# Kernel tuning notes

Measured on AMD Instinct MI355X. Metric: run time of the kernel, lower is better.

## Reference

```python
import jax, jax.numpy as jnp
import numpy as np

NUM_HEADS = 8
NUM_POINTS = 4            # sampling points per pillar point
NUM_PILLAR = 4            # points in pillar
SAMPLING_RADIUS = 0.12


def masked_softmax(logits, mask):
    # logits/mask: [B, N, H, P]; softmax over last dim, robust to fully-masked rows
    m = mask.astype(logits.dtype)
    w = jax.nn.softmax(jnp.where(mask, logits, jnp.asarray(-1e9, logits.dtype)), axis=-1) * m
    return w / jnp.clip(jnp.sum(w, axis=-1, keepdims=True), 1e-6)


def grid_sample_bilinear(feat, loc):
    # feat: [G, D, H, W]; loc: [G, Nq, P, 2] normalized to [0,1]
    # matches torch grid_sample(mode='bilinear', padding_mode='zeros', align_corners=False)
    G, D, H, W = feat.shape
    _, Nq, P, _ = loc.shape
    fm = feat.reshape(G, D, H * W).transpose(0, 2, 1)  # [G, HW, D]
    x = loc[..., 0] * W - 0.5
    y = loc[..., 1] * H - 0.5
    x0 = jnp.floor(x)
    y0 = jnp.floor(y)
    wx = x - x0
    wy = y - y0
    out = jnp.zeros((G, Nq * P, D), dtype=feat.dtype)
    corners = [(0, 0, (1 - wx) * (1 - wy)), (1, 0, wx * (1 - wy)),
               (0, 1, (1 - wx) * wy), (1, 1, wx * wy)]
    for dx, dy, w in corners:
        xi = x0 + dx
        yi = y0 + dy
        valid = (xi >= 0) & (xi < W) & (yi >= 0) & (yi < H)
        xc = jnp.clip(xi, 0, W - 1).astype(jnp.int32)
        yc = jnp.clip(yi, 0, H - 1).astype(jnp.int32)
        idx = (yc * W + xc).reshape(G, Nq * P)
        g = jnp.take_along_axis(fm, idx[:, :, None], axis=1)  # [G, Nq*P, D]
        out = out + g * (w * valid.astype(feat.dtype)).reshape(G, Nq * P, 1)
    return out.reshape(G, Nq, P, D)


def setup_inputs() -> dict:
    key = jax.random.key(0)
    ks = jax.random.split(key, 10)
    B, N, C = 1, 10000, 256
    n_cams, Himg, Wimg = 6, 60, 100
    HD = NUM_HEADS * NUM_PILLAR * NUM_POINTS  # 128
    query = jax.random.normal(ks[0], (B, N, C), jnp.float32)
    image_feats = jax.random.normal(ks[1], (B, n_cams, C, Himg, Wimg), jnp.float32)
    reference_points_cam = jax.random.uniform(ks[2], (B, n_cams, N, NUM_PILLAR, 2), jnp.float32)
    bev_mask = jax.random.bernoulli(ks[3], 0.4, (B, n_cams, N, NUM_PILLAR))
    s = 0.02
    offset_W = jax.random.normal(ks[4], (C, HD * 2), jnp.float32) * s
    offset_b = jnp.zeros((HD * 2,), jnp.float32)
    weight_W = jax.random.normal(ks[5], (C, HD), jnp.float32) * s
    weight_b = jnp.zeros((HD,), jnp.float32)
    out_W = jax.random.normal(ks[6], (C, C), jnp.float32) * s
    out_b = jnp.zeros((C,), jnp.float32)
    return {"query": query, "image_feats": image_feats,
            "reference_points_cam": reference_points_cam, "bev_mask": bev_mask,
            "offset_W": offset_W, "offset_b": offset_b,
            "weight_W": weight_W, "weight_b": weight_b,
            "out_W": out_W, "out_b": out_b}


def reference(query, image_feats, reference_points_cam, bev_mask,
              offset_W, offset_b, weight_W, weight_b, out_W, out_b):
    B, N, C = query.shape
    _, n_cams, _, Himg, Wimg = image_feats.shape
    Hh, Pp, Pn = NUM_HEADS, NUM_PILLAR, NUM_POINTS
    P = Pp * Pn
    hd = C // Hh

    offsets = jnp.tanh(query @ offset_W + offset_b) * SAMPLING_RADIUS
    offsets = offsets.reshape(B, N, Hh, Pp, Pn, 2)
    weight_logits = (query @ weight_W + weight_b).reshape(B, N, Hh, P)

    fused = jnp.zeros((B, N, C), query.dtype)
    counts = jnp.zeros((B, N), jnp.int32)
    for cam in range(n_cams):
        ref = reference_points_cam[:, cam]          # [B, N, Pp, 2]
        visible = bev_mask[:, cam]                  # [B, N, Pp]
        loc = ref[:, :, None, :, None, :] + offsets  # [B, N, H, Pp, Pn, 2]
        loc = loc.reshape(B, N, Hh, P, 2)
        vmask = jnp.broadcast_to(visible[:, :, None, :, None], (B, N, Hh, Pp, Pn)).reshape(B, N, Hh, P)
        w = masked_softmax(weight_logits, vmask)    # [B, N, H, P]
        feat = image_feats[:, cam].reshape(B * Hh, hd, Himg, Wimg)
        grid = loc.transpose(0, 2, 1, 3, 4).reshape(B * Hh, N, P, 2)
        samp = grid_sample_bilinear(feat, grid)     # [B*H, N, P, hd]
        samp = samp.reshape(B, Hh, N, P, hd).transpose(0, 2, 1, 3, 4)  # [B, N, H, P, hd]
        cam_out = jnp.sum(samp * w[..., None], axis=3).reshape(B, N, C)
        has_vis = jnp.any(visible, axis=-1)         # [B, N]
        fused = fused + cam_out * has_vis[..., None].astype(cam_out.dtype)
        counts = counts + has_vis.astype(jnp.int32)
    fused = fused / jnp.clip(counts, 1)[..., None].astype(fused.dtype)
    return fused @ out_W + out_b
```

## Files before the change

### kernel.cpp

```cpp
#include <hip/hip_runtime.h>
#include <hip/hip_bf16.h>

#define N_Q   10000
#define N_CAM 6
#define HIMG  60
#define WIMG  100
#define NPIX  6000

typedef __attribute__((ext_vector_type(4))) float f32x4;
typedef __attribute__((ext_vector_type(2))) float f32x2;
typedef __attribute__((ext_vector_type(8))) short bf16x8;

__device__ __forceinline__ unsigned short f2bf(float x) {
  __hip_bfloat16 b = __float2bfloat16(x);
  return *reinterpret_cast<unsigned short*>(&b);
}
__device__ __forceinline__ float bf2f(unsigned short u) {
  return __uint_as_float(((unsigned)u) << 16);
}
__device__ __forceinline__ float bf16lo(unsigned int u) {
  return __uint_as_float(u << 16);
}
__device__ __forceinline__ float bf16hi(unsigned int u) {
  return __uint_as_float(u & 0xffff0000u);
}
__device__ __forceinline__ void pk_fma(f32x2& acc, f32x2 a, f32x2 b) {
  asm("v_pk_fma_f32 %0, %1, %2, %0" : "+v"(acc) : "v"(a), "v"(b));
}
__device__ __forceinline__ void split8(const float* pa, bf16x8& ah, bf16x8& al) {
  const float4 v0 = *reinterpret_cast<const float4*>(pa);
  const float4 v1 = *reinterpret_cast<const float4*>(pa + 4);
  const float v[8] = {v0.x, v0.y, v0.z, v0.w, v1.x, v1.y, v1.z, v1.w};
#pragma unroll
  for (int j = 0; j < 8; ++j) {
    const unsigned short hb = f2bf(v[j]);
    ah[j] = (short)hb;
    al[j] = (short)f2bf(v[j] - bf2f(hb));
  }
}

__global__ __launch_bounds__(256) void wprep_k(
    const float* __restrict__ oW, const float* __restrict__ wW,
    const float* __restrict__ outW,
    unsigned short* __restrict__ oWth,  unsigned short* __restrict__ oWtl,
    unsigned short* __restrict__ wWth,  unsigned short* __restrict__ wWtl,
    unsigned short* __restrict__ outWth,unsigned short* __restrict__ outWtl) {
  const int b = blockIdx.x, k = threadIdx.x;
  float v; unsigned short *dh, *dl; int idx;
  if (b < 256) {
    v = oW[k * 256 + b]; dh = oWth; dl = oWtl; idx = b * 256 + k;
  } else if (b < 384) {
    int nn = b - 256; v = wW[k * 128 + nn]; dh = wWth; dl = wWtl; idx = nn * 256 + k;
  } else {
    int nn = b - 384; v = outW[k * 256 + nn]; dh = outWth; dl = outWtl; idx = nn * 256 + k;
  }
  unsigned short hv = f2bf(v);
  dh[idx] = hv;
  dl[idx] = f2bf(v - bf2f(hv));
}

__device__ __forceinline__ void gemm_bodyA32(
    const float* __restrict__ A,
    const unsigned short* __restrict__ Bh, const unsigned short* __restrict__ Bl,
    const float* __restrict__ bias, float* __restrict__ C,
    int M, int N, int mode, int bm, int bn, int tid) {
  const int l = tid & 63, w = tid >> 6;
  const int wm = w >> 1, wn = w & 1;
  const int lr = l & 15;
  const int lk = (l >> 4) * 8;

  const int am0 = min(bm + wm * 32 + lr, M - 1);
  const int am1 = min(bm + wm * 32 + 16 + lr, M - 1);
  const int bn0 = bn + wn * 32 + lr;
  const int bn1 = bn0 + 16;

  const float* pa0 = A + (size_t)am0 * 256 + lk;
  const float* pa1 = A + (size_t)am1 * 256 + lk;
  const bf16x8* pbh0 = (const bf16x8*)(Bh + (size_t)bn0 * 256 + lk);
  const bf16x8* pbh1 = (const bf16x8*)(Bh + (size_t)bn1 * 256 + lk);
  const bf16x8* pbl0 = (const bf16x8*)(Bl + (size_t)bn0 * 256 + lk);
  const bf16x8* pbl1 = (const bf16x8*)(Bl + (size_t)bn1 * 256 + lk);

  f32x4 acc00 = {}, acc01 = {}, acc10 = {}, acc11 = {};

#pragma unroll
  for (int ks = 0; ks < 8; ++ks) {
    bf16x8 ah0, al0, ah1, al1;
    split8(pa0 + ks * 32, ah0, al0);
    split8(pa1 + ks * 32, ah1, al1);
    bf16x8 bh0 = pbh0[ks * 4], bh1 = pbh1[ks * 4];
    bf16x8 bl0 = pbl0[ks * 4], bl1 = pbl1[ks * 4];
    acc00 = __builtin_amdgcn_mfma_f32_16x16x32_bf16(ah0, bh0, acc00, 0, 0, 0);
    acc00 = __builtin_amdgcn_mfma_f32_16x16x32_bf16(ah0, bl0, acc00, 0, 0, 0);
    acc00 = __builtin_amdgcn_mfma_f32_16x16x32_bf16(al0, bh0, acc00, 0, 0, 0);
    acc01 = __builtin_amdgcn_mfma_f32_16x16x32_bf16(ah0, bh1, acc01, 0, 0, 0);
    acc01 = __builtin_amdgcn_mfma_f32_16x16x32_bf16(ah0, bl1, acc01, 0, 0, 0);
    acc01 = __builtin_amdgcn_mfma_f32_16x16x32_bf16(al0, bh1, acc01, 0, 0, 0);
    acc10 = __builtin_amdgcn_mfma_f32_16x16x32_bf16(ah1, bh0, acc10, 0, 0, 0);
    acc10 = __builtin_amdgcn_mfma_f32_16x16x32_bf16(ah1, bl0, acc10, 0, 0, 0);
    acc10 = __builtin_amdgcn_mfma_f32_16x16x32_bf16(al1, bh0, acc10, 0, 0, 0);
    acc11 = __builtin_amdgcn_mfma_f32_16x16x32_bf16(ah1, bh1, acc11, 0, 0, 0);
    acc11 = __builtin_amdgcn_mfma_f32_16x16x32_bf16(ah1, bl1, acc11, 0, 0, 0);
    acc11 = __builtin_amdgcn_mfma_f32_16x16x32_bf16(al1, bh1, acc11, 0, 0, 0);
  }

  const float bias0 = bias[bn + wn * 32 + lr];
  const float bias1 = bias[bn + wn * 32 + 16 + lr];
  const int row0 = bm + wm * 32 + (l >> 4) * 4;
  const int col0 = bn + wn * 32 + lr;
#pragma unroll
  for (int r = 0; r < 4; ++r) {
    int rowA = row0 + r, rowB = row0 + 16 + r;
    float v00 = acc00[r] + bias0, v01 = acc01[r] + bias1;
    float v10 = acc10[r] + bias0, v11 = acc11[r] + bias1;
    if (mode == 1) {
      v00 = tanhf(v00) * 0.12f; v01 = tanhf(v01) * 0.12f;
      v10 = tanhf(v10) * 0.12f; v11 = tanhf(v11) * 0.12f;
    } else if (mode == 2) {
      v00 = __expf(v00); v01 = __expf(v01);
      v10 = __expf(v10); v11 = __expf(v11);
    }
    if (rowA < M) {
      C[(size_t)rowA * N + col0] = v00;
      C[(size_t)rowA * N + col0 + 16] = v01;
    }
    if (rowB < M) {
      C[(size_t)rowB * N + col0] = v10;
      C[(size_t)rowB * N + col0 + 16] = v11;
    }
  }
}

#define TRANS_BLKS (N_CAM * 94)
#define G12_BLKS   (157 * 6)

__global__ __launch_bounds__(256) void fused_prep_gemm_k(
    const float* __restrict__ in,
    const float* __restrict__ q,
    unsigned short* __restrict__ ftout,
    const unsigned short* __restrict__ B1h, const unsigned short* __restrict__ B1l,
    const float* __restrict__ b1, float* __restrict__ C1,
    const unsigned short* __restrict__ B2h, const unsigned short* __restrict__ B2l,
    const float* __restrict__ b2, float* __restrict__ C2) {
  __shared__ float tile[64][65];
  const int tid = threadIdx.x;
  if (blockIdx.x < TRANS_BLKS) {
    const int cam = blockIdx.x / 94;
    const int px0 = (blockIdx.x % 94) * 64;
    const int lpx = tid & 63;
    const int cg  = tid >> 6;
    const int px  = px0 + lpx;
    const bool pv = px < NPIX;

    for (int c0 = 0; c0 < 256; c0 += 64) {
#pragma unroll
      for (int i = 0; i < 16; ++i) {
        int cc = cg * 16 + i;
        tile[lpx][cc] = pv ? in[(cam * 256 + c0 + cc) * NPIX + px] : 0.f;
      }
      __syncthreads();
      const int wc = tid & 63;
      const int pg = tid >> 6;
#pragma unroll
      for (int i = 0; i < 16; ++i) {
        int lp = pg * 16 + i;
        int gpx = px0 + lp;
        if (gpx < NPIX)
          ftout[(size_t)(cam * NPIX + gpx) * 256 + c0 + wc] = f2bf(tile[lp][wc]);
      }
      __syncthreads();
    }
    return;
  }
  const int b  = blockIdx.x - TRANS_BLKS;
  const int bt = b % 6;
  const int bm = (b / 6) * 64;
  if (bt < 4)
    gemm_bodyA32(q, B1h, B1l, b1, C1, N_Q, 256, 1, bm, bt * 64, tid);
  else
    gemm_bodyA32(q, B2h, B2l, b2, C2, N_Q, 128, 2, bm, (bt - 4) * 64, tid);
}

__global__ __launch_bounds__(256) void sample_cam(
    const unsigned short* __restrict__ ft,
    const float* __restrict__ offs,
    const float* __restrict__ wlog,
    const float* __restrict__ refp,
    const int*   __restrict__ mask,
    unsigned short* __restrict__ partial) {
  const int tid = threadIdx.x;
  const int sub = tid >> 7;
  const int t   = tid & 127;
  const int cam = blockIdx.x / (N_Q / 2);
  const int n   = (blockIdx.x % (N_Q / 2)) * 2 + sub;
  const int h   = t >> 4;
  const int p   = t & 15;
  const int pp  = p >> 2;
  const int c   = (t >> 2) & 3;
  const int ch  = t & 3;

  const int vis = mask[(cam * N_Q + n) * 4 + pp];
  const unsigned long long bal = __ballot(vis != 0);
  if (!(bal & 0x1111ULL)) return;

  __shared__ float spt[2][1216];
  float* lds = spt[sub];
  unsigned int* ldsu = reinterpret_cast<unsigned int*>(lds);

  const float2 off = reinterpret_cast<const float2*>(offs)[n * 128 + t];
  const float E = wlog[n * 128 + t];
  const uint4* ftq2 = reinterpret_cast<const uint4*>(ft)
                      + (size_t)cam * (NPIX * 32) + (unsigned)(h * 4 + ch);

  const int abase = h * 152 + p * 9;
  const int rbase = h * 152;

  float e = vis ? E : 0.f;
  float s = e;
#pragma unroll
  for (int m = 8; m >= 1; m >>= 1)
    s += __shfl_xor(s, m, 16);
  const float wgt = e / fmaxf(s, 1e-6f);

  const float2 ref = reinterpret_cast<const float2*>(refp)[(cam * N_Q + n) * 4 + pp];
  const float x = fmaf(ref.x + off.x, (float)WIMG, -0.5f);
  const float y = fmaf(ref.y + off.y, (float)HIMG, -0.5f);
  const float x0f = floorf(x), y0f = floorf(y);
  const float wx = x - x0f, wy = y - y0f;
  const int x0 = (int)x0f, y0 = (int)y0f;
  const int x1 = x0 + 1, y1 = y0 + 1;
  const float mx0 = (x0 >= 0 && x0 < WIMG) ? 1.f : 0.f;
  const float mx1 = (x1 >= 0 && x1 < WIMG) ? 1.f : 0.f;
  const float my0 = (y0 >= 0 && y0 < HIMG) ? 1.f : 0.f;
  const float my1 = (y1 >= 0 && y1 < HIMG) ? 1.f : 0.f;
  const int xc0 = min(max(x0, 0), WIMG - 1);
  const int xc1 = min(max(x1, 0), WIMG - 1);
  const int yc0 = min(max(y0, 0), HIMG - 1);
  const int yc1 = min(max(y1, 0), HIMG - 1);
  lds[abase + 0] = (1.f - wx) * (1.f - wy) * mx0 * my0 * wgt;
  lds[abase + 1] = wx * (1.f - wy) * mx1 * my0 * wgt;
  lds[abase + 2] = (1.f - wx) * wy * mx0 * my1 * wgt;
  lds[abase + 3] = wx * wy * mx1 * my1 * wgt;
  ldsu[abase + 4] = (unsigned)(yc0 * WIMG + xc0);
  ldsu[abase + 5] = (unsigned)(yc0 * WIMG + xc1);
  ldsu[abase + 6] = (unsigned)(yc1 * WIMG + xc0);
  ldsu[abase + 7] = (unsigned)(yc1 * WIMG + xc1);
  __builtin_amdgcn_wave_barrier();

  f32x2 acc2[4] = {{0.f, 0.f}, {0.f, 0.f}, {0.f, 0.f}, {0.f, 0.f}};
  const bool pv0 = (bal      ) & 1ULL;
  const bool pv1 = (bal >>  4) & 1ULL;
  const bool pv2 = (bal >>  8) & 1ULL;
  const bool pv3 = (bal >> 12) & 1ULL;
  uint4 u0[4], u1[4], u2[4], u3[4];

#define ISSUE(U, P)                                                          \
  if (pv##P) {                                                               \
    _Pragma("unroll")                                                        \
    for (int pn = 0; pn < 4; ++pn) {                                         \
      const unsigned pix = ldsu[rbase + ((P) * 4 + pn) * 9 + 4 + c];         \
      U[pn] = ftq2[pix * 32u];                                               \
    }                                                                        \
  }
  ISSUE(u0, 0) ISSUE(u1, 1) ISSUE(u2, 2) ISSUE(u3, 3)

#define CONSUME(U, P)                                                        \
  if (pv##P) {                                                               \
    _Pragma("unroll")                                                        \
    for (int pn = 0; pn < 4; ++pn) {                                         \
      const float wv = lds[rbase + ((P) * 4 + pn) * 9 + c];                  \
      const f32x2 w2 = {wv, wv};                                             \
      f32x2 a;                                                               \
      a.x = bf16lo(U[pn].x); a.y = __uint_as_float(U[pn].x);                 \
      pk_fma(acc2[0], a, w2);                                                \
      a.x = bf16lo(U[pn].y); a.y = __uint_as_float(U[pn].y);                 \
      pk_fma(acc2[1], a, w2);                                                \
      a.x = bf16lo(U[pn].z); a.y = __uint_as_float(U[pn].z);                 \
      pk_fma(acc2[2], a, w2);                                                \
      a.x = bf16lo(U[pn].w); a.y = __uint_as_float(U[pn].w);                 \
      pk_fma(acc2[3], a, w2);                                                \
    }                                                                        \
  }
  CONSUME(u0, 0) CONSUME(u1, 1) CONSUME(u2, 2) CONSUME(u3, 3)
#undef ISSUE
#undef CONSUME

  float acc[8];
#pragma unroll
  for (int j = 0; j < 4; ++j) { acc[2 * j] = acc2[j].x; acc[2 * j + 1] = acc2[j].y; }
#pragma unroll
  for (int j = 0; j < 8; ++j) acc[j] += __shfl_xor(acc[j], 4);
#pragma unroll
  for (int j = 0; j < 8; ++j) acc[j] += __shfl_xor(acc[j], 8);

  if (c == 0) {
    unsigned w01 = (unsigned)f2bf(acc[0]) | ((unsigned)f2bf(acc[1]) << 16);
    unsigned w23 = (unsigned)f2bf(acc[2]) | ((unsigned)f2bf(acc[3]) << 16);
    unsigned w45 = (unsigned)f2bf(acc[4]) | ((unsigned)f2bf(acc[5]) << 16);
    unsigned w67 = (unsigned)f2bf(acc[6]) | ((unsigned)f2bf(acc[7]) << 16);
    uint4 v = {w01, w23, w45, w67};
    reinterpret_cast<uint4*>(partial)[((size_t)cam * N_Q + n) * 32 + h * 4 + ch] = v;
  }
}

__global__ __launch_bounds__(256) void gemm_out_k(
    const unsigned short* __restrict__ partial,
    const int*   __restrict__ mask,
    const unsigned short* __restrict__ Bh, const unsigned short* __restrict__ Bl,
    const float* __restrict__ bias, float* __restrict__ C) {
  __shared__ unsigned short Ahs[64][264];
  __shared__ unsigned short Als[64][264];
  __shared__ float    sinv[64];
  __shared__ unsigned sbits[64];

  const int tid = threadIdx.x;
  const int bm  = blockIdx.x * 64;

  if (tid < 64) {
    const int n = min(bm + tid, N_Q - 1);
    unsigned bits = 0; int cnt = 0;
#pragma unroll
    for (int cam = 0; cam < N_CAM; ++cam) {
      const int4 m4 = *reinterpret_cast<const int4*>(&mask[(cam * N_Q + n) * 4]);
      const int any = (m4.x | m4.y | m4.z | m4.w) ? 1 : 0;
      bits |= (unsigned)any << cam;
      cnt += any;
    }
    sbits[tid] = bits;
    sinv[tid]  = (cnt > 0) ? (1.f / (float)cnt) : 1.f;
  }
  __syncthreads();

  const uint4* pq = reinterpret_cast<const uint4*>(partial);
#pragma unroll
  for (int i = 0; i < 8; ++i) {
    const int u    = tid + i * 256;
    const int row  = u >> 5;
    const int slot = u & 31;
    const int n    = min(bm + row, N_Q - 1);
    const unsigned bits = sbits[row];
    const float    inv  = sinv[row];
    float v[8] = {0.f, 0.f, 0.f, 0.f, 0.f, 0.f, 0.f, 0.f};
#pragma unroll
    for (int cam = 0; cam < N_CAM; ++cam) {
      if ((bits >> cam) & 1u) {
        const uint4 x = pq[((size_t)cam * N_Q + n) * 32 + slot];
        v[0] += bf16lo(x.x); v[1] += bf16hi(x.x);
        v[2] += bf16lo(x.y); v[3] += bf16hi(x.y);
        v[4] += bf16lo(x.z); v[5] += bf16hi(x.z);
        v[6] += bf16lo(x.w); v[7] += bf16hi(x.w);
      }
    }
    unsigned short hh[8], ll[8];
#pragma unroll
    for (int j = 0; j < 8; ++j) {
      const float x = v[j] * inv;
      hh[j] = f2bf(x);
      ll[j] = f2bf(x - bf2f(hh[j]));
    }
    uint4 ph = {(unsigned)hh[0] | ((unsigned)hh[1] << 16),
                (unsigned)hh[2] | ((unsigned)hh[3] << 16),
                (unsigned)hh[4] | ((unsigned)hh[5] << 16),
                (unsigned)hh[6] | ((unsigned)hh[7] << 16)};
    uint4 pl = {(unsigned)ll[0] | ((unsigned)ll[1] << 16),
                (unsigned)ll[2] | ((unsigned)ll[3] << 16),
                (unsigned)ll[4] | ((unsigned)ll[5] << 16),
                (unsigned)ll[6] | ((unsigned)ll[7] << 16)};
    *reinterpret_cast<uint4*>(&Ahs[row][slot * 8]) = ph;
    *reinterpret_cast<uint4*>(&Als[row][slot * 8]) = pl;
  }
  __syncthreads();

  const int l  = tid & 63;
  const int w  = tid >> 6;
  const int lr = l & 15;
  const int lk = (l >> 4) * 8;

  const bf16x8* pbh[4];
  const bf16x8* pbl[4];
#pragma unroll
  for (int cf = 0; cf < 4; ++cf) {
    const int col = w * 64 + cf * 16 + lr;
    pbh[cf] = (const bf16x8*)(Bh + (size_t)col * 256 + lk);
    pbl[cf] = (const bf16x8*)(Bl + (size_t)col * 256 + lk);
  }

  f32x4 acc[4][4] = {};

#pragma unroll
  for (int ks = 0; ks < 8; ++ks) {
    bf16x8 ah[4], al[4], bh[4], bl[4];
#pragma unroll
    for (int rf = 0; rf < 4; ++rf) {
      ah[rf] = *reinterpret_cast<const bf16x8*>(&Ahs[rf * 16 + lr][ks * 32 + lk]);
      al[rf] = *reinterpret_cast<const bf16x8*>(&Als[rf * 16 + lr][ks * 32 + lk]);
    }
#pragma unroll
    for (int cf = 0; cf < 4; ++cf) {
      bh[cf] = pbh[cf][ks * 4];
      bl[cf] = pbl[cf][ks * 4];
    }
#pragma unroll
    for (int rf = 0; rf < 4; ++rf)
#pragma unroll
      for (int cf = 0; cf < 4; ++cf) {
        acc[rf][cf] = __builtin_amdgcn_mfma_f32_16x16x32_bf16(ah[rf], bh[cf], acc[rf][cf], 0, 0, 0);
        acc[rf][cf] = __builtin_amdgcn_mfma_f32_16x16x32_bf16(ah[rf], bl[cf], acc[rf][cf], 0, 0, 0);
        acc[rf][cf] = __builtin_amdgcn_mfma_f32_16x16x32_bf16(al[rf], bh[cf], acc[rf][cf], 0, 0, 0);
      }
  }

  float bias_cf[4];
#pragma unroll
  for (int cf = 0; cf < 4; ++cf) bias_cf[cf] = bias[w * 64 + cf * 16 + lr];

#pragma unroll
  for (int rf = 0; rf < 4; ++rf) {
    const int row0 = bm + rf * 16 + (l >> 4) * 4;
#pragma unroll
    for (int r = 0; r < 4; ++r) {
      const int row = row0 + r;
      if (row < N_Q) {
#pragma unroll
        for (int cf = 0; cf < 4; ++cf) {
          const int col = w * 64 + cf * 16 + lr;
          C[(size_t)row * 256 + col] = acc[rf][cf][r] + bias_cf[cf];
        }
      }
    }
  }
}

extern "C" void kernel_launch(void* const* d_in, const int* in_sizes, int n_in,
                              void* d_out, int out_size, void* d_ws, size_t ws_size,
                              hipStream_t stream) {
  const float* query = (const float*)d_in[0];
  const float* feats = (const float*)d_in[1];
  const float* refp  = (const float*)d_in[2];
  const int*   mask  = (const int*)d_in[3];
  const float* oW    = (const float*)d_in[4];
  const float* ob    = (const float*)d_in[5];
  const float* wW    = (const float*)d_in[6];
  const float* wb    = (const float*)d_in[7];
  const float* outW  = (const float*)d_in[8];
  const float* outb  = (const float*)d_in[9];
  float* out = (float*)d_out;

  char* wsb = (char*)d_ws;
  size_t o = 0;
  unsigned short* ft = (unsigned short*)(wsb + o); o += (size_t)N_CAM * NPIX * 256 * 2;
  unsigned short* oWth  = (unsigned short*)(wsb + o); o += 256 * 256 * 2;
  unsigned short* oWtl  = (unsigned short*)(wsb + o); o += 256 * 256 * 2;
  unsigned short* wWth  = (unsigned short*)(wsb + o); o += 128 * 256 * 2;
  unsigned short* wWtl  = (unsigned short*)(wsb + o); o += 128 * 256 * 2;
  unsigned short* outWth = (unsigned short*)(wsb + o); o += 256 * 256 * 2;
  unsigned short* outWtl = (unsigned short*)(wsb + o); o += 256 * 256 * 2;
  float* offs    = (float*)(wsb + o); o += (size_t)N_Q * 256 * 4;
  float* wlog    = (float*)(wsb + o); o += (size_t)N_Q * 128 * 4;
  unsigned short* partial = (unsigned short*)(wsb + o);
  o += (size_t)N_CAM * N_Q * 256 * 2;

  wprep_k<<<640, 256, 0, stream>>>(oW, wW, outW,
                                   oWth, oWtl, wWth, wWtl, outWth, outWtl);

  fused_prep_gemm_k<<<TRANS_BLKS + G12_BLKS, 256, 0, stream>>>(
      feats, query, ft, oWth, oWtl, ob, offs, wWth, wWtl, wb, wlog);

  sample_cam<<<N_CAM * (N_Q / 2), 256, 0, stream>>>(ft, offs, wlog, refp, mask,
                                                    partial);

  gemm_out_k<<<(N_Q + 63) / 64, 256, 0, stream>>>(partial, mask,
                                                  outWth, outWtl, outb, out);
}
```

Measured before the change: 147.5 us.

## Drop weight-prep kernel; split weights inline and merge offset/weight GEMM tiles

Removes the separate wprep kernel that pre-transposed and split the fp32 weights into bf16 hi/lo pairs. The GEMMs now read fp32 weights directly with strided per-element loads and split them in registers. The offset and attention-weight GEMMs are merged into a single 64-row block that computes all 384 output columns, so each query row is loaded and split once instead of six times. This saves a launch and the prep pass, but the strided uncoalesced weight loads and repeated per-block splitting add memory traffic and ALU work, and the larger 4x6 accumulator raises register pressure.

Measured after the change: 182.8 us. +23.9%, slower.

```diff
diff --git a/kernel.cpp b/kernel.cpp
--- a/kernel.cpp
+++ b/kernel.cpp
@@ -38,110 +38,26 @@
     al[j] = (short)f2bf(v[j] - bf2f(hb));
   }
 }
-
-__global__ __launch_bounds__(256) void wprep_k(
-    const float* __restrict__ oW, const float* __restrict__ wW,
-    const float* __restrict__ outW,
-    unsigned short* __restrict__ oWth,  unsigned short* __restrict__ oWtl,
-    unsigned short* __restrict__ wWth,  unsigned short* __restrict__ wWtl,
-    unsigned short* __restrict__ outWth,unsigned short* __restrict__ outWtl) {
-  const int b = blockIdx.x, k = threadIdx.x;
-  float v; unsigned short *dh, *dl; int idx;
-  if (b < 256) {
-    v = oW[k * 256 + b]; dh = oWth; dl = oWtl; idx = b * 256 + k;
-  } else if (b < 384) {
-    int nn = b - 256; v = wW[k * 128 + nn]; dh = wWth; dl = wWtl; idx = nn * 256 + k;
-  } else {
-    int nn = b - 384; v = outW[k * 256 + nn]; dh = outWth; dl = outWtl; idx = nn * 256 + k;
-  }
-  unsigned short hv = f2bf(v);
-  dh[idx] = hv;
-  dl[idx] = f2bf(v - bf2f(hv));
-}
-
-__device__ __forceinline__ void gemm_bodyA32(
-    const float* __restrict__ A,
-    const unsigned short* __restrict__ Bh, const unsigned short* __restrict__ Bl,
-    const float* __restrict__ bias, float* __restrict__ C,
-    int M, int N, int mode, int bm, int bn, int tid) {
-  const int l = tid & 63, w = tid >> 6;
-  const int wm = w >> 1, wn = w & 1;
-  const int lr = l & 15;
-  const int lk = (l >> 4) * 8;
-
-  const int am0 = min(bm + wm * 32 + lr, M - 1);
-  const int am1 = min(bm + wm * 32 + 16 + lr, M - 1);
-  const int bn0 = bn + wn * 32 + lr;
-  const int bn1 = bn0 + 16;
-
-  const float* pa0 = A + (size_t)am0 * 256 + lk;
-  const float* pa1 = A + (size_t)am1 * 256 + lk;
-  const bf16x8* pbh0 = (const bf16x8*)(Bh + (size_t)bn0 * 256 + lk);
-  const bf16x8* pbh1 = (const bf16x8*)(Bh + (size_t)bn1 * 256 + lk);
-  const bf16x8* pbl0 = (const bf16x8*)(Bl + (size_t)bn0 * 256 + lk);
-  const bf16x8* pbl1 = (const bf16x8*)(Bl + (size_t)bn1 * 256 + lk);
-
-  f32x4 acc00 = {}, acc01 = {}, acc10 = {}, acc11 = {};
-
-#pragma unroll
-  for (int ks = 0; ks < 8; ++ks) {
-    bf16x8 ah0, al0, ah1, al1;
-    split8(pa0 + ks * 32, ah0, al0);
-    split8(pa1 + ks * 32, ah1, al1);
-    bf16x8 bh0 = pbh0[ks * 4], bh1 = pbh1[ks * 4];
-    bf16x8 bl0 = pbl0[ks * 4], bl1 = pbl1[ks * 4];
-    acc00 = __builtin_amdgcn_mfma_f32_16x16x32_bf16(ah0, bh0, acc00, 0, 0, 0);
-    acc00 = __builtin_amdgcn_mfma_f32_16x16x32_bf16(ah0, bl0, acc00, 0, 0, 0);
-    acc00 = __builtin_amdgcn_mfma_f32_16x16x32_bf16(al0, bh0, acc00, 0, 0, 0);
-    acc01 = __builtin_amdgcn_mfma_f32_16x16x32_bf16(ah0, bh1, acc01, 0, 0, 0);
-    acc01 = __builtin_amdgcn_mfma_f32_16x16x32_bf16(ah0, bl1, acc01, 0, 0, 0);
-    acc01 = __builtin_amdgcn_mfma_f32_16x16x32_bf16(al0, bh1, acc01, 0, 0, 0);
-    acc10 = __builtin_amdgcn_mfma_f32_16x16x32_bf16(ah1, bh0, acc10, 0, 0, 0);
-    acc10 = __builtin_amdgcn_mfma_f32_16x16x32_bf16(ah1, bl0, acc10, 0, 0, 0);
-    acc10 = __builtin_amdgcn_mfma_f32_16x16x32_bf16(al1, bh0, acc10, 0, 0, 0);
-    acc11 = __builtin_amdgcn_mfma_f32_16x16x32_bf16(ah1, bh1, acc11, 0, 0, 0);
-    acc11 = __builtin_amdgcn_mfma_f32_16x16x32_bf16(ah1, bl1, acc11, 0, 0, 0);
-    acc11 = __builtin_amdgcn_mfma_f32_16x16x32_bf16(al1, bh1, acc11, 0, 0, 0);
-  }
-
-  const float bias0 = bias[bn + wn * 32 + lr];
-  const float bias1 = bias[bn + wn * 32 + 16 + lr];
-  const int row0 = bm + wm * 32 + (l >> 4) * 4;
-  const int col0 = bn + wn * 32 + lr;
-#pragma unroll
-  for (int r = 0; r < 4; ++r) {
-    int rowA = row0 + r, rowB = row0 + 16 + r;
-    float v00 = acc00[r] + bias0, v01 = acc01[r] + bias1;
-    float v10 = acc10[r] + bias0, v11 = acc11[r] + bias1;
-    if (mode == 1) {
-      v00 = tanhf(v00) * 0.12f; v01 = tanhf(v01) * 0.12f;
-      v10 = tanhf(v10) * 0.12f; v11 = tanhf(v11) * 0.12f;
-    } else if (mode == 2) {
-      v00 = __expf(v00); v01 = __expf(v01);
-      v10 = __expf(v10); v11 = __expf(v11);
-    }
-    if (rowA < M) {
-      C[(size_t)rowA * N + col0] = v00;
-      C[(size_t)rowA * N + col0 + 16] = v01;
-    }
-    if (rowB < M) {
-      C[(size_t)rowB * N + col0] = v10;
-      C[(size_t)rowB * N + col0 + 16] = v11;
-    }
+__device__ __forceinline__ void split8v(const float v[8], bf16x8& ah, bf16x8& al) {
+#pragma unroll
+  for (int j = 0; j < 8; ++j) {
+    const unsigned short hb = f2bf(v[j]);
+    ah[j] = (short)hb;
+    al[j] = (short)f2bf(v[j] - bf2f(hb));
   }
 }
 
 #define TRANS_BLKS (N_CAM * 94)
-#define G12_BLKS   (157 * 6)
+#define G12_BLKS   ((N_Q + 63) / 64)
 
 __global__ __launch_bounds__(256) void fused_prep_gemm_k(
     const float* __restrict__ in,
     const float* __restrict__ q,
     unsigned short* __restrict__ ftout,
-    const unsigned short* __restrict__ B1h, const unsigned short* __restrict__ B1l,
-    const float* __restrict__ b1, float* __restrict__ C1,
-    const unsigned short* __restrict__ B2h, const unsigned short* __restrict__ B2l,
-    const float* __restrict__ b2, float* __restrict__ C2) {
+    const float* __restrict__ oW, const float* __restrict__ b1,
+    float* __restrict__ C1,
+    const float* __restrict__ wW, const float* __restrict__ b2,
+    float* __restrict__ C2) {
   __shared__ float tile[64][65];
   const int tid = threadIdx.x;
   if (blockIdx.x < TRANS_BLKS) {
@@ -172,13 +88,73 @@
     }
     return;
   }
-  const int b  = blockIdx.x - TRANS_BLKS;
-  const int bt = b % 6;
-  const int bm = (b / 6) * 64;
-  if (bt < 4)
-    gemm_bodyA32(q, B1h, B1l, b1, C1, N_Q, 256, 1, bm, bt * 64, tid);
-  else
-    gemm_bodyA32(q, B2h, B2l, b2, C2, N_Q, 128, 2, bm, (bt - 4) * 64, tid);
+
+  const int bm = (blockIdx.x - TRANS_BLKS) * 64;
+  const int l  = tid & 63;
+  const int w  = tid >> 6;
+  const int lr = l & 15;
+  const int lk = (l >> 4) * 8;
+
+  const float* pa[4];
+#pragma unroll
+  for (int rf = 0; rf < 4; ++rf) {
+    const int am = min(bm + rf * 16 + lr, N_Q - 1);
+    pa[rf] = q + (size_t)am * 256 + lk;
+  }
+
+  f32x4 acc[4][6] = {};
+
+#pragma unroll
+  for (int ks = 0; ks < 8; ++ks) {
+    bf16x8 ah[4], al[4];
+#pragma unroll
+    for (int rf = 0; rf < 4; ++rf)
+      split8(pa[rf] + ks * 32, ah[rf], al[rf]);
+#pragma unroll
+    for (int cf = 0; cf < 6; ++cf) {
+      const int colu = w * 96 + cf * 16;
+      const int col  = colu + lr;
+      float bv[8];
+      if (colu < 256) {
+#pragma unroll
+        for (int j = 0; j < 8; ++j)
+          bv[j] = oW[(ks * 32 + lk + j) * 256 + col];
+      } else {
+#pragma unroll
+        for (int j = 0; j < 8; ++j)
+          bv[j] = wW[(ks * 32 + lk + j) * 128 + (col - 256)];
+      }
+      bf16x8 bh, bl;
+      split8v(bv, bh, bl);
+#pragma unroll
+      for (int rf = 0; rf < 4; ++rf) {
+        acc[rf][cf] = __builtin_amdgcn_mfma_f32_16x16x32_bf16(ah[rf], bh, acc[rf][cf], 0, 0, 0);
+        acc[rf][cf] = __builtin_amdgcn_mfma_f32_16x16x32_bf16(ah[rf], bl, acc[rf][cf], 0, 0, 0);
+        acc[rf][cf] = __builtin_amdgcn_mfma_f32_16x16x32_bf16(al[rf], bh, acc[rf][cf], 0, 0, 0);
+      }
+    }
+  }
+
+#pragma unroll
+  for (int cf = 0; cf < 6; ++cf) {
+    const int colu = w * 96 + cf * 16;
+    const int col  = colu + lr;
+    const bool isOff = colu < 256;
+    const float bs = isOff ? b1[col] : b2[col - 256];
+#pragma unroll
+    for (int rf = 0; rf < 4; ++rf) {
+      const int row0 = bm + rf * 16 + (l >> 4) * 4;
+#pragma unroll
+      for (int r = 0; r < 4; ++r) {
+        const int row = row0 + r;
+        if (row < N_Q) {
+          const float v = acc[rf][cf][r] + bs;
+          if (isOff) C1[(size_t)row * 256 + col] = tanhf(v) * 0.12f;
+          else       C2[(size_t)row * 128 + (col - 256)] = __expf(v);
+        }
+      }
+    }
+  }
 }
 
 __global__ __launch_bounds__(256) void sample_cam(
@@ -306,7 +282,7 @@
 __global__ __launch_bounds__(256) void gemm_out_k(
     const unsigned short* __restrict__ partial,
     const int*   __restrict__ mask,
-    const unsigned short* __restrict__ Bh, const unsigned short* __restrict__ Bl,
+    const float* __restrict__ outW,
     const float* __restrict__ bias, float* __restrict__ C) {
   __shared__ unsigned short Ahs[64][264];
   __shared__ unsigned short Als[64][264];
@@ -376,20 +352,11 @@
   const int lr = l & 15;
   const int lk = (l >> 4) * 8;
 
-  const bf16x8* pbh[4];
-  const bf16x8* pbl[4];
-#pragma unroll
-  for (int cf = 0; cf < 4; ++cf) {
-    const int col = w * 64 + cf * 16 + lr;
-    pbh[cf] = (const bf16x8*)(Bh + (size_t)col * 256 + lk);
-    pbl[cf] = (const bf16x8*)(Bl + (size_t)col * 256 + lk);
-  }
-
   f32x4 acc[4][4] = {};
 
 #pragma unroll
   for (int ks = 0; ks < 8; ++ks) {
-    bf16x8 ah[4], al[4], bh[4], bl[4];
+    bf16x8 ah[4], al[4];
 #pragma unroll
     for (int rf = 0; rf < 4; ++rf) {
       ah[rf] = *reinterpret_cast<const bf16x8*>(&Ahs[rf * 16 + lr][ks * 32 + lk]);
@@ -397,17 +364,20 @@
     }
 #pragma unroll
     for (int cf = 0; cf < 4; ++cf) {
-      bh[cf] = pbh[cf][ks * 4];
-      bl[cf] = pbl[cf][ks * 4];
-    }
-#pragma unroll
-    for (int rf = 0; rf < 4; ++rf)
-#pragma unroll
-      for (int cf = 0; cf < 4; ++cf) {
-        acc[rf][cf] = __builtin_amdgcn_mfma_f32_16x16x32_bf16(ah[rf], bh[cf], acc[rf][cf], 0, 0, 0);
-        acc[rf][cf] = __builtin_amdgcn_mfma_f32_16x16x32_bf16(ah[rf], bl[cf], acc[rf][cf], 0, 0, 0);
-        acc[rf][cf] = __builtin_amdgcn_mfma_f32_16x16x32_bf16(al[rf], bh[cf], acc[rf][cf], 0, 0, 0);
-      }
+      const int col = w * 64 + cf * 16 + lr;
+      float bv[8];
+#pragma unroll
+      for (int j = 0; j < 8; ++j)
+        bv[j] = outW[(ks * 32 + lk + j) * 256 + col];
+      bf16x8 bh, bl;
+      split8v(bv, bh, bl);
+#pragma unroll
+      for (int rf = 0; rf < 4; ++rf) {
+        acc[rf][cf] = __builtin_amdgcn_mfma_f32_16x16x32_bf16(ah[rf], bh, acc[rf][cf], 0, 0, 0);
+        acc[rf][cf] = __builtin_amdgcn_mfma_f32_16x16x32_bf16(ah[rf], bl, acc[rf][cf], 0, 0, 0);
+        acc[rf][cf] = __builtin_amdgcn_mfma_f32_16x16x32_bf16(al[rf], bh, acc[rf][cf], 0, 0, 0);
+      }
+    }
   }
 
   float bias_cf[4];
@@ -449,26 +419,17 @@
   char* wsb = (char*)d_ws;
   size_t o = 0;
   unsigned short* ft = (unsigned short*)(wsb + o); o += (size_t)N_CAM * NPIX * 256 * 2;
-  unsigned short* oWth  = (unsigned short*)(wsb + o); o += 256 * 256 * 2;
-  unsigned short* oWtl  = (unsigned short*)(wsb + o); o += 256 * 256 * 2;
-  unsigned short* wWth  = (unsigned short*)(wsb + o); o += 128 * 256 * 2;
-  unsigned short* wWtl  = (unsigned short*)(wsb + o); o += 128 * 256 * 2;
-  unsigned short* outWth = (unsigned short*)(wsb + o); o += 256 * 256 * 2;
-  unsigned short* outWtl = (unsigned short*)(wsb + o); o += 256 * 256 * 2;
   float* offs    = (float*)(wsb + o); o += (size_t)N_Q * 256 * 4;
   float* wlog    = (float*)(wsb + o); o += (size_t)N_Q * 128 * 4;
   unsigned short* partial = (unsigned short*)(wsb + o);
   o += (size_t)N_CAM * N_Q * 256 * 2;
 
-  wprep_k<<<640, 256, 0, stream>>>(oW, wW, outW,
-                                   oWth, oWtl, wWth, wWtl, outWth, outWtl);
-
   fused_prep_gemm_k<<<TRANS_BLKS + G12_BLKS, 256, 0, stream>>>(
-      feats, query, ft, oWth, oWtl, ob, offs, wWth, wWtl, wb, wlog);
+      feats, query, ft, oW, ob, offs, wW, wb, wlog);
 
   sample_cam<<<N_CAM * (N_Q / 2), 256, 0, stream>>>(ft, offs, wlog, refp, mask,
                                                     partial);
 
   gemm_out_k<<<(N_Q + 63) / 64, 256, 0, stream>>>(partial, mask,
-                                                  outWth, outWtl, outb, out);
-}
+                                                  outW, outb, out);
+}
```
